# Performance work log

Measured on AMD Instinct MI355X. Metric: run time of the kernel, lower is better.

Reference implementation:

```python
import jax, jax.numpy as jnp
import numpy as np

B, C, L, D = 8, 32, 2048, 128
R, H = 8, 4  # num_routers, num_heads


def setup_inputs() -> dict:
    key = jax.random.key(0)
    ks = jax.random.split(key, 20)
    p = lambda k, shape: jax.random.normal(k, shape, dtype=jnp.float32) * 0.02
    inp = {
        "Z": jax.random.normal(ks[0], (B, C, L, D), dtype=jnp.float32),
        "router": p(ks[1], (R, D)),
        # router_sender projections (d_model -> d_model, torch Linear stored as x@W+b)
        "Wq1": p(ks[2], (D, D)), "bq1": jnp.zeros((D,), jnp.float32),
        "Wk1": p(ks[3], (D, D)), "bk1": jnp.zeros((D,), jnp.float32),
        "Wv1": p(ks[4], (D, D)), "bv1": jnp.zeros((D,), jnp.float32),
        "Wo1": p(ks[5], (D, D)), "bo1": jnp.zeros((D,), jnp.float32),
        # router_receiver projections
        "Wq2": p(ks[6], (D, D)), "bq2": jnp.zeros((D,), jnp.float32),
        "Wk2": p(ks[7], (D, D)), "bk2": jnp.zeros((D,), jnp.float32),
        "Wv2": p(ks[8], (D, D)), "bv2": jnp.zeros((D,), jnp.float32),
        "Wo2": p(ks[9], (D, D)), "bo2": jnp.zeros((D,), jnp.float32),
        # LayerNorm
        "gamma": jnp.ones((D,), jnp.float32),
        "beta": jnp.zeros((D,), jnp.float32),
    }
    return inp


def _cross_attn(q_in, k_in, v_in, Wq, bq, Wk, bk, Wv, bv, Wo, bo):
    # Informer FullAttention + AttentionLayer (dropout=0)
    Bn, Lq, Dm = q_in.shape
    Lk = k_in.shape[1]
    dh = Dm // H
    q = (q_in @ Wq + bq).reshape(Bn, Lq, H, dh)
    k = (k_in @ Wk + bk).reshape(Bn, Lk, H, dh)
    v = (v_in @ Wv + bv).reshape(Bn, Lk, H, dh)
    scale = 1.0 / np.sqrt(dh)
    scores = jnp.einsum("blhe,bshe->bhls", q, k) * scale
    A = jax.nn.softmax(scores, axis=-1)
    out = jnp.einsum("bhls,bshd->blhd", A, v).reshape(Bn, Lq, Dm)
    return out @ Wo + bo


def _layernorm(x, gamma, beta, eps=1e-5):
    mu = jnp.mean(x, axis=-1, keepdims=True)
    var = jnp.mean(jnp.square(x - mu), axis=-1, keepdims=True)
    return (x - mu) * jax.lax.rsqrt(var + eps) * gamma + beta


def reference(Z, router, Wq1, bq1, Wk1, bk1, Wv1, bv1, Wo1, bo1,
              Wq2, bq2, Wk2, bk2, Wv2, bv2, Wo2, bo2, gamma, beta):
    Bz, Cz, Lz, Dz = Z.shape
    x = Z.reshape(Bz * Cz, Lz, Dz)
    batch_router = jnp.broadcast_to(router[None], (Bz * Cz, R, Dz))
    # stage 1: routers attend to the sequence (R x L)
    router_buffer = _cross_attn(batch_router, x, x,
                                Wq1, bq1, Wk1, bk1, Wv1, bv1, Wo1, bo1)
    # stage 2: sequence attends to routers (L x R)
    router_receive = _cross_attn(x, router_buffer, router_buffer,
                                 Wq2, bq2, Wk2, bk2, Wv2, bv2, Wo2, bo2)
    out = _layernorm(x + router_receive, gamma, beta)
    return out.reshape(Bz, Cz, Lz, Dz)
```

## Files before the change

kernel.cpp:

```cpp
#include <hip/hip_runtime.h>

typedef float f4_t __attribute__((ext_vector_type(4)));
typedef __bf16 bf8_t __attribute__((ext_vector_type(8)));
typedef __bf16 bf4_t __attribute__((ext_vector_type(4)));

#define MFMA16(a,b,c) __builtin_amdgcn_mfma_f32_16x16x32_bf16((a),(b),(c),0,0,0)

static constexpr float kScale = 0.17677669529663687f;

__global__ __launch_bounds__(256) void k0_fold(
    const float* __restrict__ router, const float* __restrict__ Wq1,
    const float* __restrict__ bq1, const float* __restrict__ Wk1,
    const float* __restrict__ bk1, __bf16* __restrict__ q1t,
    float* __restrict__ c1)
{
  __shared__ float q1[8][128];
  const int t = threadIdx.x;
  for (int idx = t; idx < 1024; idx += 256) {
    int r = idx >> 7, dp = idx & 127;
    float acc = bq1[dp];
    for (int e = 0; e < 128; ++e) acc += router[r*128 + e] * Wq1[e*128 + dp];
    q1[r][dp] = acc;
  }
  __syncthreads();
  for (int idx = t; idx < 4096; idx += 256) {
    int j = idx >> 7, e = idx & 127;
    int h = j >> 3, r = j & 7;
    float acc = 0.f;
    for (int d = 0; d < 32; ++d) acc += q1[r][h*32 + d] * Wk1[e*128 + h*32 + d];
    q1t[idx] = (__bf16)(acc * kScale);
  }
  if (t < 32) {
    int h = t >> 3, r = t & 7;
    float acc = 0.f;
    for (int d = 0; d < 32; ++d) acc += q1[r][h*32 + d] * bk1[h*32 + d];
    c1[t] = acc * kScale;
  }
}

__global__ __launch_bounds__(512) void k1_stage1(
    const float* __restrict__ Z, const __bf16* __restrict__ q1t_g,
    const float* __restrict__ c1_g, float* __restrict__ xap,
    float* __restrict__ lp)
{
  __shared__ __bf16 xb[64][136];
  __shared__ __bf16 xT[128][72];
  __shared__ __bf16 PT[32][72];
  __shared__ __bf16 q1t[32][136];
  __shared__ float lds_l[32];

  const int tid = threadIdx.x;
  const int bid = blockIdx.x;
  const float* xbase = Z + (size_t)bid * (1024 * 128);

  {
    int j = tid >> 4, e0 = (tid & 15) << 3;
    *(uint4*)&q1t[j][e0] = *(const uint4*)(q1t_g + j*128 + e0);
  }
  if (tid < 32) lds_l[tid] = 0.f;

  const int lane = tid & 63;
  const int w = tid >> 6;
  const int lc = lane & 15;
  const int lg = lane >> 4;
  const int ms = w >> 2;
  const int ns = w & 3;
  float c1v[4];
#pragma unroll
  for (int r2 = 0; r2 < 4; ++r2) c1v[r2] = c1_g[ms*16 + lg*4 + r2];

  const f4_t fzero = {0.f, 0.f, 0.f, 0.f};
  f4_t accxa[2] = { fzero, fzero };
  float Lacc[4] = {0.f, 0.f, 0.f, 0.f};

  __syncthreads();

  for (int tile = 0; tile < 16; ++tile) {
    const float* xt = xbase + tile * (64 * 128);
#pragma unroll
    for (int i = 0; i < 4; ++i) {
      int f = tid + i*512;
      int pos = f >> 5, d0 = (f & 31) << 2;
      f4_t v = __builtin_nontemporal_load((const f4_t*)(xt + pos*128 + d0));
      bf4_t b4 = { (__bf16)v.x, (__bf16)v.y, (__bf16)v.z, (__bf16)v.w };
      *(bf4_t*)&xb[pos][d0] = b4;
    }
    __syncthreads();
#pragma unroll
    for (int s = 0; s < 2; ++s) {
      int u = tid + s*512;
      int dim = u & 127, pb = (u >> 7) << 3;
      bf8_t t8;
#pragma unroll
      for (int p = 0; p < 8; ++p) t8[p] = xb[pb + p][dim];
      *(bf8_t*)&xT[dim][pb] = t8;
    }
    f4_t sacc = fzero;
#pragma unroll
    for (int ks = 0; ks < 4; ++ks) {
      bf8_t a = *(const bf8_t*)&q1t[ms*16 + lc][ks*32 + lg*8];
      bf8_t b = *(const bf8_t*)&xb[ns*16 + lc][ks*32 + lg*8];
      sacc = MFMA16(a, b, sacc);
    }
    const int posn = ns*16 + lc;
#pragma unroll
    for (int r2 = 0; r2 < 4; ++r2) {
      float p = __expf(sacc[r2] + c1v[r2]);
      Lacc[r2] += p;
      PT[ms*16 + lg*4 + r2][posn] = (__bf16)p;
    }
    __syncthreads();
#pragma unroll
    for (int nt = 0; nt < 2; ++nt) {
      const int dimt = (ns << 1) + nt;
#pragma unroll
      for (int ks = 0; ks < 2; ++ks) {
        bf8_t a = *(const bf8_t*)&PT[ms*16 + lc][ks*32 + lg*8];
        bf8_t b = *(const bf8_t*)&xT[dimt*16 + lc][ks*32 + lg*8];
        accxa[nt] = MFMA16(a, b, accxa[nt]);
      }
    }
    __syncthreads();
  }

#pragma unroll
  for (int r2 = 0; r2 < 4; ++r2) {
    float v = Lacc[r2];
    v += __shfl_xor(v, 1);
    v += __shfl_xor(v, 2);
    v += __shfl_xor(v, 4);
    v += __shfl_xor(v, 8);
    if (lc == 0) atomicAdd(&lds_l[ms*16 + lg*4 + r2], v);
  }
  __syncthreads();

  float* xo = xap + (size_t)bid * 4096;
#pragma unroll
  for (int nt = 0; nt < 2; ++nt) {
    const int dim = ((ns << 1) + nt)*16 + lc;
#pragma unroll
    for (int r2 = 0; r2 < 4; ++r2) {
      int j = ms*16 + lg*4 + r2;
      xo[j*128 + dim] = accxa[nt][r2];
    }
  }
  if (tid < 32) lp[bid*32 + tid] = lds_l[tid];
}

__global__ __launch_bounds__(256) void k1b_mid(
    const float* __restrict__ xap, const float* __restrict__ lp,
    const float* __restrict__ Wv1, const float* __restrict__ bv1,
    const float* __restrict__ Wo1, const float* __restrict__ bo1,
    const float* __restrict__ Wk2, const float* __restrict__ bk2,
    const float* __restrict__ Wv2, const float* __restrict__ bv2,
    const float* __restrict__ Wq2, const float* __restrict__ bq2,
    const float* __restrict__ Wo2,
    __bf16* __restrict__ kt2, float* __restrict__ c2, __bf16* __restrict__ vt2)
{
  __shared__ float xa[32][129];
  __shared__ float invl[32];
  __shared__ float out1[8][128];
  __shared__ float rb[8][128];
  __shared__ float k2s[8][128];
  __shared__ float v2s[8][128];

  const int t = threadIdx.x, b = blockIdx.x;
  const float* p0 = xap + (size_t)(b*2) * 4096;
  const float* p1 = xap + (size_t)(b*2 + 1) * 4096;
  for (int idx = t; idx < 4096; idx += 256)
    xa[idx >> 7][idx & 127] = p0[idx] + p1[idx];
  if (t < 32) invl[t] = 1.f / (lp[b*64 + t] + lp[b*64 + 32 + t]);
  __syncthreads();

  for (int idx = t; idx < 1024; idx += 256) {
    int r = idx >> 7, hd = idx & 127, h = hd >> 5;
    int j = h*8 + r;
    float acc = 0.f;
    for (int e = 0; e < 128; ++e) acc += xa[j][e] * Wv1[e*128 + hd];
    out1[r][hd] = acc * invl[j] + bv1[hd];
  }
  __syncthreads();
  for (int idx = t; idx < 1024; idx += 256) {
    int r = idx >> 7, e2 = idx & 127;
    float acc = bo1[e2];
    for (int hd = 0; hd < 128; ++hd) acc += out1[r][hd] * Wo1[hd*128 + e2];
    rb[r][e2] = acc;
  }
  __syncthreads();
  for (int idx = t; idx < 2048; idx += 256) {
    int sel = idx >> 10;
    int r = (idx >> 7) & 7, hd = idx & 127;
    const float* W = sel ? Wv2 : Wk2;
    const float* bb = sel ? bv2 : bk2;
    float acc = bb[hd];
    for (int e = 0; e < 128; ++e) acc += rb[r][e] * W[e*128 + hd];
    float (*dst)[128] = sel ? v2s : k2s;
    dst[r][hd] = acc;
  }
  __syncthreads();
  for (int idx = t; idx < 4096; idx += 256) {
    int j = idx >> 7, e = idx & 127;
    int h = j >> 3, r = j & 7;
    float acck = 0.f, accv = 0.f;
    for (int d = 0; d < 32; ++d) {
      acck += Wq2[e*128 + h*32 + d] * k2s[r][h*32 + d];
      accv += v2s[r][h*32 + d] * Wo2[(h*32 + d)*128 + e];
    }
    kt2[(size_t)b*4096 + j*128 + e] = (__bf16)(acck * kScale);
    vt2[(size_t)b*4096 + e*32 + j] = (__bf16)accv;
  }
  if (t < 32) {
    int h = t >> 3, r = t & 7;
    float acc = 0.f;
    for (int d = 0; d < 32; ++d) acc += bq2[h*32 + d] * k2s[r][h*32 + d];
    c2[b*32 + t] = acc * kScale;
  }
}

__global__ __launch_bounds__(256, 4) void k2_stage2(
    const float* __restrict__ Z, const __bf16* __restrict__ kt2,
    const float* __restrict__ c2g, const __bf16* __restrict__ vt2,
    const float* __restrict__ bo2, const float* __restrict__ gamma,
    const float* __restrict__ beta, float* __restrict__ out)
{
  __shared__ __bf16 xb[64][136];
  __shared__ __bf16 P2[64][56];

  const int tid = threadIdx.x;
  const int bid = blockIdx.x;
  const int batch = bid >> 5;
  const size_t rowbase = (size_t)bid * (64 * 128);
  const float* x = Z + rowbase;
  float* y = out + rowbase;

  const __bf16* ktb = kt2 + (size_t)batch * 4096;
  const __bf16* vtb = vt2 + (size_t)batch * 4096;

  const int lane = tid & 63;
  const int w = tid >> 6;
  const int lc = lane & 15;
  const int lg = lane >> 4;
  const int arow = w*16 + lc;

  const f4_t fzero = {0.f, 0.f, 0.f, 0.f};

  f4_t sacc[2] = { fzero, fzero };
#pragma unroll
  for (int ks = 0; ks < 4; ++ks) {
    const float* xp = x + arow*128 + ks*32 + lg*8;
    f4_t v0 = *(const f4_t*)xp;
    f4_t v1 = *(const f4_t*)(xp + 4);
    bf8_t a = { (__bf16)v0.x, (__bf16)v0.y, (__bf16)v0.z, (__bf16)v0.w,
                (__bf16)v1.x, (__bf16)v1.y, (__bf16)v1.z, (__bf16)v1.w };
    *(bf8_t*)&xb[arow][ks*32 + lg*8] = a;
#pragma unroll
    for (int nt = 0; nt < 2; ++nt) {
      bf8_t b = *(const bf8_t*)(ktb + (nt*16 + lc)*128 + ks*32 + lg*8);
      sacc[nt] = MFMA16(a, b, sacc[nt]);
    }
  }
  float c2v[2] = { c2g[batch*32 + lc], c2g[batch*32 + 16 + lc] };
#pragma unroll
  for (int nt = 0; nt < 2; ++nt) {
#pragma unroll
    for (int r2 = 0; r2 < 4; ++r2) {
      float s = sacc[nt][r2] + c2v[nt];
      float m = s;
      m = fmaxf(m, __shfl_xor(m, 1));
      m = fmaxf(m, __shfl_xor(m, 2));
      m = fmaxf(m, __shfl_xor(m, 4));
      float p = __expf(s - m);
      float sum = p;
      sum += __shfl_xor(sum, 1);
      sum += __shfl_xor(sum, 2);
      sum += __shfl_xor(sum, 4);
      P2[w*16 + lg*4 + r2][nt*16 + lc] = (__bf16)(p / sum);
    }
  }

  bf8_t pa = *(const bf8_t*)&P2[w*16 + lc][lg*8];
  f4_t racc[8];
#pragma unroll
  for (int nt = 0; nt < 8; ++nt) {
    bf8_t b = *(const bf8_t*)(vtb + (nt*16 + lc)*32 + lg*8);
    racc[nt] = MFMA16(pa, b, fzero);
  }

  float bo2v[8], gv[8], bv[8];
#pragma unroll
  for (int nt = 0; nt < 8; ++nt) {
    int dd = nt*16 + lc;
    bo2v[nt] = bo2[dd]; gv[nt] = gamma[dd]; bv[nt] = beta[dd];
  }
#pragma unroll
  for (int r2 = 0; r2 < 4; ++r2) {
    int pos = w*16 + lg*4 + r2;
    float vv[8];
    float s1 = 0.f, s2 = 0.f;
#pragma unroll
    for (int nt = 0; nt < 8; ++nt) {
      float xv = (float)xb[pos][nt*16 + lc];
      float tv = racc[nt][r2] + bo2v[nt] + xv;
      vv[nt] = tv; s1 += tv; s2 += tv*tv;
    }
    s1 += __shfl_xor(s1, 1); s1 += __shfl_xor(s1, 2);
    s1 += __shfl_xor(s1, 4); s1 += __shfl_xor(s1, 8);
    s2 += __shfl_xor(s2, 1); s2 += __shfl_xor(s2, 2);
    s2 += __shfl_xor(s2, 4); s2 += __shfl_xor(s2, 8);
    float mean = s1 * (1.f/128.f);
    float var = s2 * (1.f/128.f) - mean*mean;
    float rstd = rsqrtf(var + 1e-5f);
#pragma unroll
    for (int nt = 0; nt < 8; ++nt)
      __builtin_nontemporal_store((vv[nt] - mean) * rstd * gv[nt] + bv[nt],
                                  &y[pos*128 + nt*16 + lc]);
  }
}

extern "C" void kernel_launch(void* const* d_in, const int* in_sizes, int n_in,
                              void* d_out, int out_size, void* d_ws, size_t ws_size,
                              hipStream_t stream)
{
  const float* Z     = (const float*)d_in[0];
  const float* router= (const float*)d_in[1];
  const float* Wq1   = (const float*)d_in[2];
  const float* bq1   = (const float*)d_in[3];
  const float* Wk1   = (const float*)d_in[4];
  const float* bk1   = (const float*)d_in[5];
  const float* Wv1   = (const float*)d_in[6];
  const float* bv1   = (const float*)d_in[7];
  const float* Wo1   = (const float*)d_in[8];
  const float* bo1   = (const float*)d_in[9];
  const float* Wq2   = (const float*)d_in[10];
  const float* bq2   = (const float*)d_in[11];
  const float* Wk2   = (const float*)d_in[12];
  const float* bk2   = (const float*)d_in[13];
  const float* Wv2   = (const float*)d_in[14];
  const float* bv2   = (const float*)d_in[15];
  const float* Wo2   = (const float*)d_in[16];
  const float* bo2   = (const float*)d_in[17];
  const float* gamma = (const float*)d_in[18];
  const float* beta  = (const float*)d_in[19];
  float* out = (float*)d_out;

  char* base = (char*)d_ws;
  __bf16* q1tb = (__bf16*)base;
  float*  c1   = (float*)(base + 8192);
  float*  c2   = (float*)(base + 8448);
  float*  lp   = (float*)(base + 41216);
  float*  xap  = (float*)(base + 131072);
  __bf16* kt2b = (__bf16*)(base + 131072 + 8388608);
  __bf16* vt2b = (__bf16*)(base + 131072 + 8388608 + 2097152);
  (void)in_sizes; (void)n_in; (void)out_size; (void)ws_size;

  k0_fold<<<dim3(1), dim3(256), 0, stream>>>(router, Wq1, bq1, Wk1, bk1, q1tb, c1);
  k1_stage1<<<dim3(512), dim3(512), 0, stream>>>(Z, q1tb, c1, xap, lp);
  k1b_mid<<<dim3(256), dim3(256), 0, stream>>>(xap, lp, Wv1, bv1, Wo1, bo1,
                                               Wk2, bk2, Wv2, bv2, Wq2, bq2, Wo2,
                                               kt2b, c2, vt2b);
  k2_stage2<<<dim3(8192), dim3(256), 0, stream>>>(Z, kt2b, c2, vt2b, bo2, gamma, beta, out);
}
```

Baseline: 321.4 us.

## Cache bf16 copy of input in stage1 and split stage1 across more blocks

Stage1 now also writes the bf16-converted input tile to a workspace buffer. Stage2 reads that buffer instead of re-reading and converting fp32 Z. Stage1 is split into 2048 blocks of 256 rows, giving 8 partial sums per sequence; the mid kernel now reduces these. The q1t operand is held in registers instead of LDS. Stage2 moves to 512-thread blocks of 128 rows. Total DRAM traffic stays similar, since the bf16 write is added while the stage2 read is halved, so any gain depends on better stage1 parallelism and on cache hits for the bf16 copy.

```diff
diff --git a/kernel.cpp b/kernel.cpp
--- a/kernel.cpp
+++ b/kernel.cpp
@@ -41,22 +41,18 @@
 __global__ __launch_bounds__(512) void k1_stage1(
     const float* __restrict__ Z, const __bf16* __restrict__ q1t_g,
     const float* __restrict__ c1_g, float* __restrict__ xap,
-    float* __restrict__ lp)
+    float* __restrict__ lp, __bf16* __restrict__ xws)
 {
   __shared__ __bf16 xb[64][136];
   __shared__ __bf16 xT[128][72];
   __shared__ __bf16 PT[32][72];
-  __shared__ __bf16 q1t[32][136];
   __shared__ float lds_l[32];
 
   const int tid = threadIdx.x;
   const int bid = blockIdx.x;
-  const float* xbase = Z + (size_t)bid * (1024 * 128);
-
-  {
-    int j = tid >> 4, e0 = (tid & 15) << 3;
-    *(uint4*)&q1t[j][e0] = *(const uint4*)(q1t_g + j*128 + e0);
-  }
+  const float* xbase = Z + (size_t)bid * (256 * 128);
+  __bf16* xwb = xws + (size_t)bid * (256 * 128);
+
   if (tid < 32) lds_l[tid] = 0.f;
 
   const int lane = tid & 63;
@@ -68,6 +64,10 @@
   float c1v[4];
 #pragma unroll
   for (int r2 = 0; r2 < 4; ++r2) c1v[r2] = c1_g[ms*16 + lg*4 + r2];
+  bf8_t aq[4];
+#pragma unroll
+  for (int ks = 0; ks < 4; ++ks)
+    aq[ks] = *(const bf8_t*)(q1t_g + (ms*16 + lc)*128 + ks*32 + lg*8);
 
   const f4_t fzero = {0.f, 0.f, 0.f, 0.f};
   f4_t accxa[2] = { fzero, fzero };
@@ -75,7 +75,7 @@
 
   __syncthreads();
 
-  for (int tile = 0; tile < 16; ++tile) {
+  for (int tile = 0; tile < 4; ++tile) {
     const float* xt = xbase + tile * (64 * 128);
 #pragma unroll
     for (int i = 0; i < 4; ++i) {
@@ -84,6 +84,7 @@
       f4_t v = __builtin_nontemporal_load((const f4_t*)(xt + pos*128 + d0));
       bf4_t b4 = { (__bf16)v.x, (__bf16)v.y, (__bf16)v.z, (__bf16)v.w };
       *(bf4_t*)&xb[pos][d0] = b4;
+      *(bf4_t*)(xwb + (tile*64 + pos)*128 + d0) = b4;
     }
     __syncthreads();
 #pragma unroll
@@ -98,9 +99,8 @@
     f4_t sacc = fzero;
 #pragma unroll
     for (int ks = 0; ks < 4; ++ks) {
-      bf8_t a = *(const bf8_t*)&q1t[ms*16 + lc][ks*32 + lg*8];
       bf8_t b = *(const bf8_t*)&xb[ns*16 + lc][ks*32 + lg*8];
-      sacc = MFMA16(a, b, sacc);
+      sacc = MFMA16(aq[ks], b, sacc);
     }
     const int posn = ns*16 + lc;
 #pragma unroll
@@ -165,11 +165,19 @@
   __shared__ float v2s[8][128];
 
   const int t = threadIdx.x, b = blockIdx.x;
-  const float* p0 = xap + (size_t)(b*2) * 4096;
-  const float* p1 = xap + (size_t)(b*2 + 1) * 4096;
-  for (int idx = t; idx < 4096; idx += 256)
-    xa[idx >> 7][idx & 127] = p0[idx] + p1[idx];
-  if (t < 32) invl[t] = 1.f / (lp[b*64 + t] + lp[b*64 + 32 + t]);
+  for (int idx = t; idx < 4096; idx += 256) {
+    float s = 0.f;
+#pragma unroll
+    for (int k = 0; k < 8; ++k)
+      s += xap[(size_t)(b*8 + k) * 4096 + idx];
+    xa[idx >> 7][idx & 127] = s;
+  }
+  if (t < 32) {
+    float s = 0.f;
+#pragma unroll
+    for (int k = 0; k < 8; ++k) s += lp[(b*8 + k)*32 + t];
+    invl[t] = 1.f / s;
+  }
   __syncthreads();
 
   for (int idx = t; idx < 1024; idx += 256) {
@@ -217,21 +225,20 @@
   }
 }
 
-__global__ __launch_bounds__(256, 4) void k2_stage2(
-    const float* __restrict__ Z, const __bf16* __restrict__ kt2,
+__global__ __launch_bounds__(512) void k2_stage2(
+    const __bf16* __restrict__ xws, const __bf16* __restrict__ kt2,
     const float* __restrict__ c2g, const __bf16* __restrict__ vt2,
     const float* __restrict__ bo2, const float* __restrict__ gamma,
     const float* __restrict__ beta, float* __restrict__ out)
 {
-  __shared__ __bf16 xb[64][136];
-  __shared__ __bf16 P2[64][56];
+  __shared__ __bf16 xb[128][136];
+  __shared__ __bf16 P2[128][40];
 
   const int tid = threadIdx.x;
   const int bid = blockIdx.x;
-  const int batch = bid >> 5;
-  const size_t rowbase = (size_t)bid * (64 * 128);
-  const float* x = Z + rowbase;
-  float* y = out + rowbase;
+  const int batch = bid >> 4;
+  const __bf16* xsrc = xws + (size_t)bid * (128 * 128);
+  float* y = out + (size_t)bid * (128 * 128);
 
   const __bf16* ktb = kt2 + (size_t)batch * 4096;
   const __bf16* vtb = vt2 + (size_t)batch * 4096;
@@ -240,19 +247,21 @@
   const int w = tid >> 6;
   const int lc = lane & 15;
   const int lg = lane >> 4;
-  const int arow = w*16 + lc;
+
+#pragma unroll
+  for (int j = 0; j < 4; ++j) {
+    int c = lane + j*64;
+    int pos = w*16 + (c >> 4);
+    int d0 = (c & 15) << 3;
+    *(uint4*)&xb[pos][d0] = *(const uint4*)(xsrc + pos*128 + d0);
+  }
 
   const f4_t fzero = {0.f, 0.f, 0.f, 0.f};
 
   f4_t sacc[2] = { fzero, fzero };
 #pragma unroll
   for (int ks = 0; ks < 4; ++ks) {
-    const float* xp = x + arow*128 + ks*32 + lg*8;
-    f4_t v0 = *(const f4_t*)xp;
-    f4_t v1 = *(const f4_t*)(xp + 4);
-    bf8_t a = { (__bf16)v0.x, (__bf16)v0.y, (__bf16)v0.z, (__bf16)v0.w,
-                (__bf16)v1.x, (__bf16)v1.y, (__bf16)v1.z, (__bf16)v1.w };
-    *(bf8_t*)&xb[arow][ks*32 + lg*8] = a;
+    bf8_t a = *(const bf8_t*)&xb[w*16 + lc][ks*32 + lg*8];
 #pragma unroll
     for (int nt = 0; nt < 2; ++nt) {
       bf8_t b = *(const bf8_t*)(ktb + (nt*16 + lc)*128 + ks*32 + lg*8);
@@ -344,19 +353,20 @@
   float* out = (float*)d_out;
 
   char* base = (char*)d_ws;
-  __bf16* q1tb = (__bf16*)base;
+  __bf16* q1tb = (__bf16*)(base);
   float*  c1   = (float*)(base + 8192);
-  float*  c2   = (float*)(base + 8448);
-  float*  lp   = (float*)(base + 41216);
-  float*  xap  = (float*)(base + 131072);
-  __bf16* kt2b = (__bf16*)(base + 131072 + 8388608);
-  __bf16* vt2b = (__bf16*)(base + 131072 + 8388608 + 2097152);
+  float*  c2   = (float*)(base + 16384);
+  float*  lp   = (float*)(base + 65536);
+  float*  xap  = (float*)(base + (1u<<20));
+  __bf16* kt2b = (__bf16*)(base + (36u<<20));
+  __bf16* vt2b = (__bf16*)(base + (38u<<20));
+  __bf16* xws  = (__bf16*)(base + (40u<<20));
   (void)in_sizes; (void)n_in; (void)out_size; (void)ws_size;
 
   k0_fold<<<dim3(1), dim3(256), 0, stream>>>(router, Wq1, bq1, Wk1, bk1, q1tb, c1);
-  k1_stage1<<<dim3(512), dim3(512), 0, stream>>>(Z, q1tb, c1, xap, lp);
+  k1_stage1<<<dim3(2048), dim3(512), 0, stream>>>(Z, q1tb, c1, xap, lp, xws);
   k1b_mid<<<dim3(256), dim3(256), 0, stream>>>(xap, lp, Wv1, bv1, Wo1, bo1,
                                                Wk2, bk2, Wv2, bv2, Wq2, bq2, Wo2,
                                                kt2b, c2, vt2b);
-  k2_stage2<<<dim3(8192), dim3(256), 0, stream>>>(Z, kt2b, c2, vt2b, bo2, gamma, beta, out);
-}
+  k2_stage2<<<dim3(4096), dim3(512), 0, stream>>>(xws, kt2b, c2, vt2b, bo2, gamma, beta, out);
+}
```

After: 291.5 us. 9.3% less time.
